# Performance work log

Measured on AMD Instinct MI355X. Metric: run time of the kernel, lower is better.

## Reference

```python
import jax, jax.numpy as jnp
import numpy as np

N = 100000      # nodes
E = 1600000     # edges (without self loops)
G = 64          # graphs in batch
H = 4           # attention heads
C = 42          # hidden dim per head (node_hidden_dim)
DIN = 42        # node_input_dim
NEG_SLOPE = 0.2  # PyG GATConv default


def setup_inputs() -> dict:
    key = jax.random.key(0)
    ks = jax.random.split(key, 24)
    x = jax.random.normal(ks[0], (N, DIN), jnp.float32)
    # edges with src != dst (GATConv removes then re-adds self loops; we emulate
    # by generating loop-free edges and appending self loops in reference())
    src = jax.random.randint(ks[1], (E,), 0, N, dtype=jnp.int32)
    off = jax.random.randint(ks[2], (E,), 1, N, dtype=jnp.int32)
    dst = ((src + off) % N).astype(jnp.int32)
    edge_index = jnp.stack([src, dst])
    batch = jnp.sort(jax.random.randint(ks[3], (N,), 0, G, dtype=jnp.int32))
    s = 0.1
    inp = {
        'x': x, 'edge_index': edge_index, 'batch': batch,
        'lin0_w': s * jax.random.normal(ks[4], (DIN, C), jnp.float32),
        'lin0_b': jnp.zeros((C,), jnp.float32),
    }
    ins = [C, H * C, H * C]  # layer input widths: 42, 168, 168
    for l in range(3):
        inp[f'W{l+1}'] = s * jax.random.normal(ks[5 + 4 * l], (ins[l], H * C), jnp.float32)
        inp[f'asrc{l+1}'] = s * jax.random.normal(ks[6 + 4 * l], (H, C), jnp.float32)
        inp[f'adst{l+1}'] = s * jax.random.normal(ks[7 + 4 * l], (H, C), jnp.float32)
        inp[f'b{l+1}'] = jnp.zeros((H * C,), jnp.float32)
    return inp


def _gat_layer(x, src, dst, W, a_src, a_dst, bias):
    # x: [N, Fin] -> h: [N, H, C]
    h = (x @ W).reshape(N, H, C)
    alpha_src = jnp.sum(h * a_src[None], axis=-1)  # [N, H]
    alpha_dst = jnp.sum(h * a_dst[None], axis=-1)  # [N, H]
    e = jax.nn.leaky_relu(alpha_src[src] + alpha_dst[dst], NEG_SLOPE)  # [E', H]
    # segment softmax over incoming edges of each destination node
    m = jax.ops.segment_max(e, dst, num_segments=N)
    m = jnp.where(jnp.isfinite(m), m, 0.0)
    ex = jnp.exp(e - m[dst])
    denom = jax.ops.segment_sum(ex, dst, num_segments=N)
    alpha = ex / denom[dst]  # self loops guarantee denom > 0
    out = jax.ops.segment_sum(h[src] * alpha[:, :, None], dst, num_segments=N)
    return out.reshape(N, H * C) + bias


def reference(x, edge_index, batch, lin0_w, lin0_b,
              W1, asrc1, adst1, b1,
              W2, asrc2, adst2, b2,
              W3, asrc3, adst3, b3):
    x = jax.nn.elu(x @ lin0_w + lin0_b)
    loops = jnp.arange(N, dtype=edge_index.dtype)
    src = jnp.concatenate([edge_index[0], loops])
    dst = jnp.concatenate([edge_index[1], loops])
    for W, a_s, a_d, b in ((W1, asrc1, adst1, b1),
                           (W2, asrc2, adst2, b2),
                           (W3, asrc3, adst3, b3)):
        x = jax.nn.elu(_gat_layer(x, src, dst, W, a_s, a_d, b))
        # dropout p=0.0 -> identity; residual in original is computed but unused
    counts = jax.ops.segment_sum(jnp.ones((N,), x.dtype), batch, num_segments=G)
    sums = jax.ops.segment_sum(x, batch, num_segments=G)
    return sums / jnp.maximum(counts, 1.0)[:, None]  # [G, H*C]
```

## Files before the change

kernel.cpp:

```cpp
#include <hip/hip_runtime.h>
#include <hip/hip_fp16.h>
#include <cstdint>

#define HC 168
#define CC 42
#define NH 4
#define PH 44
#define HP 176
#define HPB 352
#define AP 192
#define A0P 64
#define NEG 0.2f

typedef _Float16 f16;
typedef __attribute__((ext_vector_type(8))) _Float16 f16x8;
typedef __attribute__((ext_vector_type(4))) float f32x4;

__device__ __forceinline__ float lrelu(float v) { return fmaxf(v, NEG * v); }
__device__ __forceinline__ float eluf(float v)  { return v > 0.f ? v : __expf(v) - 1.f; }

__device__ __forceinline__ float sel4(float4 w, int h) {
  float r = w.x;
  r = (h == 1) ? w.y : r;
  r = (h == 2) ? w.z : r;
  r = (h == 3) ? w.w : r;
  return r;
}

__device__ __forceinline__ void wconv_item(
    const float* __restrict__ W, f16* __restrict__ Wf, int i,
    int KCN, int kpad, int Fink, int cpad, int Ncols, int wstride) {
  int lane = i & 63;
  int t = i >> 6;
  int kc = t % KCN;
  int ct = t / KCN;
  int cl = ct * 16 + (lane & 15);
  int corig; bool cok;
  if (cpad) { int h = cl / PH, c = cl % PH; cok = (c < CC && h < NH); corig = h * CC + c; }
  else      { cok = (cl < Ncols); corig = cl; }
  f16 vals[8];
#pragma unroll
  for (int j = 0; j < 8; ++j) {
    int kp = kc * 32 + (lane >> 4) * 8 + j;
    int korig; bool kok;
    if (kpad) { int h = kp / PH, c = kp % PH; kok = (c < CC && h < NH && kp < HP); korig = h * CC + c; }
    else      { kok = (kp < Fink); korig = kp; }
    vals[j] = (kok && cok) ? (f16)W[korig * wstride + corig] : (f16)0.f;
  }
  *(f16x8*)(Wf + (size_t)i * 8) = *(f16x8*)vals;
}

__global__ void prep_kernel(
    const float* __restrict__ lin0_w,
    const float* __restrict__ W1, const float* __restrict__ W2, const float* __restrict__ W3,
    const float* __restrict__ as1, const float* __restrict__ ad1,
    const float* __restrict__ as2, const float* __restrict__ ad2,
    const float* __restrict__ as3, const float* __restrict__ ad3,
    f16* __restrict__ Wf0, f16* __restrict__ Wf1, f16* __restrict__ Wf2, f16* __restrict__ Wf3,
    float* __restrict__ aPad,
    int* __restrict__ cursor, float* __restrict__ sums,
    int N, int G) {
  const int W0N = 4 * 2 * 64, W1N = 11 * 2 * 64, W2N = 11 * 6 * 64;
  int i = blockIdx.x * 256 + threadIdx.x;
  if (i < N) { cursor[i] = 0; return; }
  i -= N;
  if (i < G * HC) { sums[i] = 0.f; return; }
  i -= G * HC;
  if (i < 3 * 2 * 176) {
    int l = i / 352, rem = i % 352, which = rem / 176, col = rem % 176;
    const float* tabs[6] = {as1, ad1, as2, ad2, as3, ad3};
    const float* tab = tabs[l * 2 + which];
    int h = col / PH, c = col % PH;
    aPad[i] = (c < CC) ? tab[h * CC + c] : 0.f;
    return;
  }
  i -= 3 * 2 * 176;
  if (i < W0N) { wconv_item(lin0_w, Wf0, i, 2, 0, CC, 0, CC, CC); return; }
  i -= W0N;
  if (i < W1N) { wconv_item(W1, Wf1, i, 2, 0, CC, 1, HC, HC); return; }
  i -= W1N;
  if (i < W2N) { wconv_item(W2, Wf2, i, 6, 1, HC, 1, HC, HC); return; }
  i -= W2N;
  if (i < W2N) { wconv_item(W3, Wf3, i, 6, 1, HC, 1, HC, HC); return; }
}

__global__ __launch_bounds__(256) void mfma_gemm0_kernel(
    const float* __restrict__ X, const f16* __restrict__ Wf,
    const float* __restrict__ bias, f16* __restrict__ Out, int N) {
  const int lane = threadIdx.x & 63;
  const int wid = (blockIdx.x * 256 + threadIdx.x) >> 6;
  const int row0 = wid * 16;
  if (row0 >= N) return;
  const int r = lane & 15, g = lane >> 4;
  f16x8 a[2];
  const float* xp = X + (int64_t)(row0 + r) * CC;
#pragma unroll
  for (int kc = 0; kc < 2; ++kc) {
#pragma unroll
    for (int j = 0; j < 8; ++j) {
      int k = kc * 32 + g * 8 + j;
      a[kc][j] = (k < CC) ? (f16)xp[k] : (f16)0.f;
    }
  }
  f16* op = Out + (int64_t)row0 * A0P;
#pragma unroll
  for (int ct = 0; ct < 4; ++ct) {
    f32x4 acc = {0.f, 0.f, 0.f, 0.f};
#pragma unroll
    for (int kc = 0; kc < 2; ++kc) {
      f16x8 b = *(const f16x8*)(Wf + (((size_t)ct * 2 + kc) * 64 + lane) * 8);
      acc = __builtin_amdgcn_mfma_f32_16x16x32_f16(a[kc], b, acc, 0, 0, 0);
    }
    const int col = ct * 16 + r;
    float bv = (col < CC) ? bias[col] : 0.f;
#pragma unroll
    for (int v = 0; v < 4; ++v) {
      f16 o = (col < CC) ? (f16)eluf(acc[v] + bv) : (f16)0.f;
      op[(int64_t)(g * 4 + v) * A0P + col] = o;
    }
  }
}

template<int KCN>
__global__ __launch_bounds__(256) void mfma_gemmL_kernel(
    const f16* __restrict__ A, const f16* __restrict__ Wf,
    const float* __restrict__ asP, const float* __restrict__ adP,
    f16* __restrict__ Out, float4* __restrict__ as4, float4* __restrict__ ad4,
    int N) {
  const int lane = threadIdx.x & 63;
  const int wid = (blockIdx.x * 256 + threadIdx.x) >> 6;
  const int row0 = wid * 16;
  if (row0 >= N) return;
  const int r = lane & 15, g = lane >> 4;
  f16x8 a[KCN];
  const f16* ap = A + (int64_t)(row0 + r) * (KCN * 32) + g * 8;
#pragma unroll
  for (int kc = 0; kc < KCN; ++kc) a[kc] = *(const f16x8*)(ap + kc * 32);
  f16* op = Out + (int64_t)row0 * HP;
  float psA[4][4], psD[4][4];
#pragma unroll
  for (int h = 0; h < 4; ++h)
#pragma unroll
    for (int v = 0; v < 4; ++v) { psA[h][v] = 0.f; psD[h][v] = 0.f; }

#pragma unroll
  for (int ct = 0; ct < 11; ++ct) {
    f32x4 acc = {0.f, 0.f, 0.f, 0.f};
#pragma unroll
    for (int kc = 0; kc < KCN; ++kc) {
      f16x8 b = *(const f16x8*)(Wf + (((size_t)ct * KCN + kc) * 64 + lane) * 8);
      acc = __builtin_amdgcn_mfma_f32_16x16x32_f16(a[kc], b, acc, 0, 0, 0);
    }
    const int col = ct * 16 + r;
    const float aS = asP[col], aD = adP[col];
    const int hlo = (ct * 16) / PH;
    const bool hi = (col >= (hlo + 1) * PH);
#pragma unroll
    for (int v = 0; v < 4; ++v) {
      f16 hq = (f16)acc[v];
      op[(int64_t)(g * 4 + v) * HP + col] = hq;
      float hf = (float)hq;
      float tA = hf * aS, tD = hf * aD;
      psA[hlo][v] += hi ? 0.f : tA;
      psD[hlo][v] += hi ? 0.f : tD;
      if (hlo < 3) {
        psA[hlo + 1][v] += hi ? tA : 0.f;
        psD[hlo + 1][v] += hi ? tD : 0.f;
      }
    }
  }
#pragma unroll
  for (int h = 0; h < 4; ++h)
#pragma unroll
    for (int v = 0; v < 4; ++v) {
      float aa = psA[h][v], dd = psD[h][v];
#pragma unroll
      for (int m = 1; m < 16; m <<= 1) {
        aa += __shfl_xor(aa, m, 64);
        dd += __shfl_xor(dd, m, 64);
      }
      psA[h][v] = aa; psD[h][v] = dd;
    }
  if (r < 4) {
    int row = row0 + g * 4 + r;
    as4[row] = make_float4(psA[0][r], psA[1][r], psA[2][r], psA[3][r]);
  } else if (r < 8) {
    int rr = r - 4;
    int row = row0 + g * 4 + rr;
    ad4[row] = make_float4(psD[0][rr], psD[1][rr], psD[2][rr], psD[3][rr]);
  }
}

__global__ void hist_kernel(const int* __restrict__ dst, int* __restrict__ cnt, int E) {
  int e = blockIdx.x * 256 + threadIdx.x;
  if (e < E) atomicAdd(&cnt[dst[e]], 1);
}

__global__ __launch_bounds__(256) void scan1_kernel(
    const int* __restrict__ cnt, int* __restrict__ rp1, int* __restrict__ blksum, int N) {
  __shared__ int lds[256];
  int t = threadIdx.x;
  int base = blockIdx.x * 1024 + t * 4;
  int v0 = (base + 0 < N) ? cnt[base + 0] : 0;
  int v1 = (base + 1 < N) ? cnt[base + 1] : 0;
  int v2 = (base + 2 < N) ? cnt[base + 2] : 0;
  int v3 = (base + 3 < N) ? cnt[base + 3] : 0;
  v1 += v0; v2 += v1; v3 += v2;
  lds[t] = v3;
  __syncthreads();
  for (int off = 1; off < 256; off <<= 1) {
    int add = (t >= off) ? lds[t - off] : 0;
    __syncthreads();
    lds[t] += add;
    __syncthreads();
  }
  int excl = lds[t] - v3;
  if (base + 0 < N) rp1[base + 0] = excl + v0;
  if (base + 1 < N) rp1[base + 1] = excl + v1;
  if (base + 2 < N) rp1[base + 2] = excl + v2;
  if (base + 3 < N) rp1[base + 3] = excl + v3;
  if (t == 255) blksum[blockIdx.x] = lds[255];
}

__global__ __launch_bounds__(256) void scan2_kernel(int* __restrict__ blksum, int nblk) {
  __shared__ int lds[256];
  int t = threadIdx.x;
  int v = (t < nblk) ? blksum[t] : 0;
  lds[t] = v;
  __syncthreads();
  for (int off = 1; off < 256; off <<= 1) {
    int add = (t >= off) ? lds[t - off] : 0;
    __syncthreads();
    lds[t] += add;
    __syncthreads();
  }
  if (t < nblk) blksum[t] = lds[t] - v;
}

__global__ void scan3_kernel(const int* __restrict__ blksum, int* __restrict__ rp1,
                             int* __restrict__ row_ptr0, int* __restrict__ cnt_cursor, int N) {
  int i = blockIdx.x * 256 + threadIdx.x;
  if (i >= N) return;
  int incl = rp1[i] + blksum[i >> 10];
  rp1[i] = incl;
  cnt_cursor[i] = incl - cnt_cursor[i];
  if (i == 0) row_ptr0[0] = 0;
}

__global__ void scatter_gbound_kernel(
    const int* __restrict__ src, const int* __restrict__ dst,
    int* __restrict__ cursor, int* __restrict__ src_sorted,
    const int* __restrict__ batch, int* __restrict__ gstart,
    int E, int N, int G) {
  int i = blockIdx.x * 256 + threadIdx.x;
  if (i <= N) {
    if (i == 0) {
      for (int g = 0; g <= batch[0]; ++g) gstart[g] = 0;
    } else if (i == N) {
      for (int g = batch[N - 1] + 1; g <= G; ++g) gstart[g] = N;
    } else {
      int a = batch[i - 1], b = batch[i];
      for (int g = a + 1; g <= b; ++g) gstart[g] = i;
    }
  }
  if (i < E) {
    int pos = atomicAdd(&cursor[dst[i]], 1);
    src_sorted[pos] = src[i];
  }
}

__global__ __launch_bounds__(256) void gat_agg_kernel(
    const int* __restrict__ row_ptr, const int* __restrict__ src_sorted,
    const f16* __restrict__ H16, const float4* __restrict__ as4,
    const float4* __restrict__ ad4_, const float* __restrict__ bias,
    f16* __restrict__ out, int N) {
  __shared__ int   loff[4][64];
  __shared__ float lw4[4][64][4];
  const int wv = threadIdx.x >> 6;
  const int lane = threadIdx.x & 63;
  const int wid = (blockIdx.x * 256 + threadIdx.x) >> 6;
  if (wid >= N) return;
  const int n = wid;
  const bool act = (lane < 44);
  const int hL = act ? (lane / 11) : 0;
  const int myoff = lane * 8;
  const float4 adn = ad4_[n];
  float ax = 0.f, ay = 0.f, az = 0.f, aw = 0.f, den = 0.f;

#define GAT_ACC(boff_, w_)                                                  \
  {                                                                         \
    den += w_;                                                              \
    if (act) {                                                              \
      float2 raw = *(const float2*)((const char*)H16 + (boff_) + myoff);    \
      __half2 u0 = *(__half2*)&raw.x, u1 = *(__half2*)&raw.y;               \
      float2 f0 = __half22float2(u0), f1 = __half22float2(u1);              \
      ax += f0.x * w_; ay += f0.y * w_;                                     \
      az += f1.x * w_; aw += f1.y * w_;                                     \
    }                                                                       \
  }

  {
    const float4 a4 = as4[n];
    float4 w4 = make_float4(__expf(lrelu(a4.x + adn.x)), __expf(lrelu(a4.y + adn.y)),
                            __expf(lrelu(a4.z + adn.z)), __expf(lrelu(a4.w + adn.w)));
    float w = sel4(w4, hL);
    GAT_ACC((int64_t)n * HPB, w);
  }

  const int beg = row_ptr[n], end = row_ptr[n + 1];
  for (int base = beg; base < end; base += 64) {
    const int m = min(64, end - base);
    int idx = (lane < m) ? src_sorted[base + lane] : n;
    float4 a4 = as4[idx];
    float4 w4 = make_float4(__expf(lrelu(a4.x + adn.x)), __expf(lrelu(a4.y + adn.y)),
                            __expf(lrelu(a4.z + adn.z)), __expf(lrelu(a4.w + adn.w)));
    loff[wv][lane] = idx * HPB;
    *(float4*)&lw4[wv][lane][0] = w4;

#define GAT_EDGE(jj)                                                        \
    {                                                                       \
      int boff = loff[wv][jj];                                              \
      float w = lw4[wv][jj][hL];                                            \
      GAT_ACC((int64_t)boff, w);                                            \
    }

    int j = 0;
    for (; j + 8 <= m; j += 8) {
      GAT_EDGE(j)     GAT_EDGE(j + 1) GAT_EDGE(j + 2) GAT_EDGE(j + 3)
      GAT_EDGE(j + 4) GAT_EDGE(j + 5) GAT_EDGE(j + 6) GAT_EDGE(j + 7)
    }
    for (; j < m; ++j) GAT_EDGE(j)
#undef GAT_EDGE
  }
#undef GAT_ACC

  if (lane < 48) {
    f16 o[4] = {(f16)0.f, (f16)0.f, (f16)0.f, (f16)0.f};
    if (act) {
      const int q = lane - hL * 11;
      const float acc[4] = {ax, ay, az, aw};
      const float rden = 1.f / den;
#pragma unroll
      for (int t = 0; t < 4; ++t) {
        int c = q * 4 + t;
        if (c < CC) o[t] = (f16)eluf(acc[t] * rden + bias[hL * CC + c]);
      }
    }
    *(uint2*)(out + (int64_t)n * AP + lane * 4) = *(uint2*)o;
  }
}

#define PSPLIT 4
__global__ __launch_bounds__(192) void pool2_kernel(
    const f16* __restrict__ x, const int* __restrict__ gstart,
    float* __restrict__ sums, int G) {
  int g = blockIdx.x;
  int t = threadIdx.x;
  if (t >= HC) return;
  int pos = (t / CC) * PH + t % CC;
  int beg = gstart[g], end = gstart[g + 1];
  float s = 0.f;
  for (int n = beg + (int)blockIdx.y; n < end; n += PSPLIT)
    s += (float)x[(int64_t)n * AP + pos];
  atomicAdd(sums + g * HC + t, s);
}

__global__ void out2_kernel(const float* __restrict__ sums, const int* __restrict__ gstart,
                            float* __restrict__ out, int G) {
  int i = blockIdx.x * 256 + threadIdx.x;
  if (i >= G * HC) return;
  int g = i / HC;
  float cnt = (float)(gstart[g + 1] - gstart[g]);
  out[i] = sums[i] / fmaxf(cnt, 1.f);
}

static inline int cdiv(int64_t a, int b) { return (int)((a + b - 1) / b); }

extern "C" void kernel_launch(void* const* d_in, const int* in_sizes, int n_in,
                              void* d_out, int out_size, void* d_ws, size_t ws_size,
                              hipStream_t stream) {
  const float* x      = (const float*)d_in[0];
  const int*   eidx   = (const int*)d_in[1];
  const int*   batch  = (const int*)d_in[2];
  const float* lin0_w = (const float*)d_in[3];
  const float* lin0_b = (const float*)d_in[4];
  const float* W[3]  = {(const float*)d_in[5],  (const float*)d_in[9],  (const float*)d_in[13]};
  const float* As[3] = {(const float*)d_in[6],  (const float*)d_in[10], (const float*)d_in[14]};
  const float* Ad[3] = {(const float*)d_in[7],  (const float*)d_in[11], (const float*)d_in[15]};
  const float* Bi[3] = {(const float*)d_in[8],  (const float*)d_in[12], (const float*)d_in[16]};

  const int N = in_sizes[2];
  const int E = in_sizes[1] / 2;
  const int G = out_size / HC;
  const int* src = eidx;
  const int* dst = eidx + E;

  char* p = (char*)d_ws;
  f16* act0 = (f16*)p;  p += (size_t)N * A0P * 2;
  f16* actv = (f16*)p;  p += (size_t)N * AP * 2;
  f16* h16  = (f16*)p;  p += (size_t)N * HP * 2;
  f16* Wf0  = (f16*)p;  p += (size_t)4 * 2 * 64 * 8 * 2;
  f16* Wf1  = (f16*)p;  p += (size_t)11 * 2 * 64 * 8 * 2;
  f16* Wf2  = (f16*)p;  p += (size_t)11 * 6 * 64 * 8 * 2;
  f16* Wf3  = (f16*)p;  p += (size_t)11 * 6 * 64 * 8 * 2;
  float* aPad = (float*)p; p += (size_t)3 * 2 * 176 * 4;
  float* as_  = (float*)p; p += (size_t)N * NH * 4;
  float* ad_  = (float*)p; p += (size_t)N * NH * 4;
  float* sums = (float*)p; p += (size_t)G * HC * 4;
  int* gstart     = (int*)p; p += (size_t)(G + 1) * 4;
  int* row_ptr    = (int*)p; p += (size_t)(N + 1) * 4;
  int* cursor     = (int*)p; p += (size_t)N * 4;
  int* blksum     = (int*)p; p += 256 * 4;
  int* src_sorted = (int*)p; p += (size_t)E * 4;
  (void)ws_size;

  const int nblk = cdiv(N, 1024);
  const int mfma_blocks = cdiv(cdiv(N, 16), 4);

  {
    int tot = N + G * HC + 3 * 2 * 176 + 4 * 2 * 64 + 11 * 2 * 64 + 2 * (11 * 6 * 64);
    prep_kernel<<<cdiv(tot, 256), 256, 0, stream>>>(
        lin0_w, W[0], W[1], W[2], As[0], Ad[0], As[1], Ad[1], As[2], Ad[2],
        Wf0, Wf1, Wf2, Wf3, aPad, cursor, sums, N, G);
  }

  mfma_gemm0_kernel<<<mfma_blocks, 256, 0, stream>>>(x, Wf0, lin0_b, act0, N);

  hist_kernel<<<cdiv(E, 256), 256, 0, stream>>>(dst, cursor, E);
  scan1_kernel<<<nblk, 256, 0, stream>>>(cursor, row_ptr + 1, blksum, N);
  scan2_kernel<<<1, 256, 0, stream>>>(blksum, nblk);
  scan3_kernel<<<cdiv(N, 256), 256, 0, stream>>>(blksum, row_ptr + 1, row_ptr, cursor, N);
  scatter_gbound_kernel<<<cdiv(E > N + 1 ? E : N + 1, 256), 256, 0, stream>>>(
      src, dst, cursor, src_sorted, batch, gstart, E, N, G);

  for (int l = 0; l < 3; ++l) {
    const float* asP = aPad + l * 352;
    const float* adP = aPad + l * 352 + 176;
    if (l == 0)
      mfma_gemmL_kernel<2><<<mfma_blocks, 256, 0, stream>>>(
          act0, Wf1, asP, adP, h16, (float4*)as_, (float4*)ad_, N);
    else
      mfma_gemmL_kernel<6><<<mfma_blocks, 256, 0, stream>>>(
          actv, (l == 1) ? Wf2 : Wf3, asP, adP, h16, (float4*)as_, (float4*)ad_, N);
    gat_agg_kernel<<<cdiv(N, 4), 256, 0, stream>>>(
        row_ptr, src_sorted, h16, (const float4*)as_, (const float4*)ad_, Bi[l], actv, N);
  }

  pool2_kernel<<<dim3(G, PSPLIT), 192, 0, stream>>>(actv, gstart, sums, G);
  out2_kernel<<<cdiv(G * HC, 256), 256, 0, stream>>>(sums, gstart, (float*)d_out, G);
}
```

Measured before the change: 894.2 us.

## Partition histogram and scatter atomics by destination range across passes

The histogram and the CSR scatter kernels now launch NPASS times as many blocks. Each block handles one destination-node range, so that at any moment the atomics and scattered writes of concurrent blocks land in a narrower address window and get better cache locality. The cost is that every block re-reads dst (and src) for all edges, which multiplies index traffic by eight. Pool2 is also split over more blocks (PSPLIT from 4 to 16) to give it more parallelism.

```diff
diff --git a/kernel.cpp b/kernel.cpp
--- a/kernel.cpp
+++ b/kernel.cpp
@@ -11,6 +11,7 @@
 #define AP 192
 #define A0P 64
 #define NEG 0.2f
+#define NPASS 8
 
 typedef _Float16 f16;
 typedef __attribute__((ext_vector_type(8))) _Float16 f16x8;
@@ -191,9 +192,15 @@
   }
 }
 
-__global__ void hist_kernel(const int* __restrict__ dst, int* __restrict__ cnt, int E) {
-  int e = blockIdx.x * 256 + threadIdx.x;
-  if (e < E) atomicAdd(&cnt[dst[e]], 1);
+__global__ void hist_kernel(const int* __restrict__ dst, int* __restrict__ cnt,
+                            int E, int N) {
+  int pass = blockIdx.x & (NPASS - 1);
+  int e = (blockIdx.x >> 3) * 256 + threadIdx.x;
+  if (e >= E) return;
+  int d = dst[e];
+  int lo = (int)((int64_t)pass * N / NPASS);
+  int hi = (int)((int64_t)(pass + 1) * N / NPASS);
+  if (d >= lo && d < hi) atomicAdd(&cnt[d], 1);
 }
 
 __global__ __launch_bounds__(256) void scan1_kernel(
@@ -252,8 +259,9 @@
     int* __restrict__ cursor, int* __restrict__ src_sorted,
     const int* __restrict__ batch, int* __restrict__ gstart,
     int E, int N, int G) {
-  int i = blockIdx.x * 256 + threadIdx.x;
-  if (i <= N) {
+  int pass = blockIdx.x & (NPASS - 1);
+  int i = (blockIdx.x >> 3) * 256 + threadIdx.x;
+  if (pass == 0 && i <= N) {
     if (i == 0) {
       for (int g = 0; g <= batch[0]; ++g) gstart[g] = 0;
     } else if (i == N) {
@@ -264,8 +272,13 @@
     }
   }
   if (i < E) {
-    int pos = atomicAdd(&cursor[dst[i]], 1);
-    src_sorted[pos] = src[i];
+    int d = dst[i];
+    int lo = (int)((int64_t)pass * N / NPASS);
+    int hi = (int)((int64_t)(pass + 1) * N / NPASS);
+    if (d >= lo && d < hi) {
+      int pos = atomicAdd(&cursor[d], 1);
+      src_sorted[pos] = src[i];
+    }
   }
 }
 
@@ -350,7 +363,7 @@
   }
 }
 
-#define PSPLIT 4
+#define PSPLIT 16
 __global__ __launch_bounds__(192) void pool2_kernel(
     const f16* __restrict__ x, const int* __restrict__ gstart,
     float* __restrict__ sums, int G) {
@@ -426,12 +439,15 @@
 
   mfma_gemm0_kernel<<<mfma_blocks, 256, 0, stream>>>(x, Wf0, lin0_b, act0, N);
 
-  hist_kernel<<<cdiv(E, 256), 256, 0, stream>>>(dst, cursor, E);
+  hist_kernel<<<cdiv(E, 256) * NPASS, 256, 0, stream>>>(dst, cursor, E, N);
   scan1_kernel<<<nblk, 256, 0, stream>>>(cursor, row_ptr + 1, blksum, N);
   scan2_kernel<<<1, 256, 0, stream>>>(blksum, nblk);
   scan3_kernel<<<cdiv(N, 256), 256, 0, stream>>>(blksum, row_ptr + 1, row_ptr, cursor, N);
-  scatter_gbound_kernel<<<cdiv(E > N + 1 ? E : N + 1, 256), 256, 0, stream>>>(
-      src, dst, cursor, src_sorted, batch, gstart, E, N, G);
+  {
+    int nx = cdiv(E > N + 1 ? E : N + 1, 256) * NPASS;
+    scatter_gbound_kernel<<<nx, 256, 0, stream>>>(
+        src, dst, cursor, src_sorted, batch, gstart, E, N, G);
+  }
 
   for (int l = 0; l < 3; ++l) {
     const float* asP = aPad + l * 352;
```

Result: faster. 775.2 us (median of 2 runs) (-13.3%).
